# Kernel optimization log

Hardware: AMD Instinct MI355X
Metric: run time of the kernel (lower is better)

## Reference

```python
import jax, jax.numpy as jnp
import numpy as np

B, N, DIM = 4, 2048, 512
HEADS, DIM_HEAD = 8, 64
INNER = HEADS * DIM_HEAD  # 512
EPS = 1e-5
SCALE = DIM_HEAD ** -0.5


def _layernorm(x, g):
    # matches custom LayerNorm: unbiased=False var, no bias term
    mean = jnp.mean(x, axis=-1, keepdims=True)
    var = jnp.var(x, axis=-1, keepdims=True)
    return (x - mean) * jax.lax.rsqrt(var + EPS) * g


def setup_inputs() -> dict:
    key = jax.random.key(0)
    ks = jax.random.split(key, 6)
    x = jax.random.normal(ks[0], (B, N, DIM), dtype=jnp.float32)
    attn_bias = jax.random.normal(ks[1], (HEADS, N, N), dtype=jnp.float32)
    w_q = jax.random.normal(ks[2], (DIM, INNER), dtype=jnp.float32) * 0.02
    w_kv = jax.random.normal(ks[3], (DIM, 2 * DIM_HEAD), dtype=jnp.float32) * 0.02
    w_out = jax.random.normal(ks[4], (INNER, DIM), dtype=jnp.float32) * 0.02
    g_in = jnp.ones((DIM,), dtype=jnp.float32)
    g_out = jnp.ones((DIM,), dtype=jnp.float32)
    return {"x": x, "attn_bias": attn_bias, "w_q": w_q, "w_kv": w_kv,
            "w_out": w_out, "g_in": g_in, "g_out": g_out}


def reference(x, attn_bias, w_q, w_kv, w_out, g_in, g_out):
    b, n, _ = x.shape
    xn = _layernorm(x, g_in)                                  # [b, n, dim]
    q = (xn @ w_q).reshape(b, n, HEADS, DIM_HEAD)
    q = jnp.transpose(q, (0, 2, 1, 3)) * SCALE                # [b, h, n, d]
    kv = xn @ w_kv                                            # [b, n, 2d]
    k, v = jnp.split(kv, 2, axis=-1)                          # each [b, n, d] (multi-query)
    sim = jnp.einsum('bhid,bjd->bhij', q, k) + attn_bias      # [b, h, n, n]
    attn = jax.nn.softmax(sim, axis=-1)
    out = jnp.einsum('bhij,bjd->bhid', attn, v)               # [b, h, n, d]
    out = jnp.transpose(out, (0, 2, 1, 3)).reshape(b, n, INNER)
    out = out @ w_out                                         # [b, n, dim]
    return _layernorm(out, g_out)
```

## Files before the change

### kernel.cpp

```cpp
#include <hip/hip_runtime.h>
#include <hip/hip_bf16.h>

#define B_ 4
#define N_ 2048
#define DIM_ 512
#define HEADS_ 8
#define DHEAD_ 64
#define EPS_ 1e-5f
#define SCALE_ 0.125f

typedef __attribute__((ext_vector_type(8))) short short8;
typedef __attribute__((ext_vector_type(4))) float f32x4;
#define MFMA16(a, b, c) __builtin_amdgcn_mfma_f32_16x16x32_bf16(a, b, c, 0, 0, 0)

__device__ __forceinline__ float bf2f(__hip_bfloat16 v) { return __bfloat162float(v); }
__device__ __forceinline__ float us2f(unsigned short u) {
    __hip_bfloat16 h; *(unsigned short*)&h = u; return bf2f(h);
}
__device__ __forceinline__ float load_in(const void* p, size_t i, int isf32) {
    if (isf32) return ((const float*)p)[i];
    return bf2f(((const __hip_bfloat16*)p)[i]);
}

__device__ __forceinline__ void gload_lds16(const void* g, void* l) {
    __builtin_amdgcn_global_load_lds((const __attribute__((address_space(1))) void*)g,
                                     (__attribute__((address_space(3))) void*)l, 16, 0, 0);
}

__global__ void detect_kernel(const unsigned int* __restrict__ g, int* __restrict__ flag) {
    if (threadIdx.x == 0 && blockIdx.x == 0)
        *flag = (*g == 0x3F800000u) ? 1 : 0;
}

__global__ __launch_bounds__(256) void transpose_w(const void* __restrict__ w,
                                                   __hip_bfloat16* __restrict__ wt,
                                                   int K, int N, const int* __restrict__ flag) {
    int isf32 = *flag;
    int idx = blockIdx.x * 256 + threadIdx.x;
    if (idx >= K * N) return;
    int k = idx / N, n = idx % N;
    wt[(size_t)n * K + k] = __float2bfloat16(load_in(w, idx, isf32));
}

__global__ __launch_bounds__(256) void ln1_kernel(const void* __restrict__ x,
                                                  const void* __restrict__ g,
                                                  __hip_bfloat16* __restrict__ out,
                                                  const int* __restrict__ flag) {
    int isf32 = *flag;
    int row = blockIdx.x;
    int tid = threadIdx.x;
    size_t base = (size_t)row * DIM_;
    float v0 = load_in(x, base + tid, isf32);
    float v1 = load_in(x, base + tid + 256, isf32);
    float s = v0 + v1;
    float sq = v0 * v0 + v1 * v1;
    for (int off = 32; off > 0; off >>= 1) {
        s += __shfl_xor(s, off, 64);
        sq += __shfl_xor(sq, off, 64);
    }
    __shared__ float ls[4], lq[4];
    int wid = tid >> 6;
    if ((tid & 63) == 0) { ls[wid] = s; lq[wid] = sq; }
    __syncthreads();
    s = ls[0] + ls[1] + ls[2] + ls[3];
    sq = lq[0] + lq[1] + lq[2] + lq[3];
    float mean = s * (1.0f / DIM_);
    float var = sq * (1.0f / DIM_) - mean * mean;
    float rstd = rsqrtf(var + EPS_);
    out[base + tid]       = __float2bfloat16((v0 - mean) * rstd * load_in(g, tid, isf32));
    out[base + tid + 256] = __float2bfloat16((v1 - mean) * rstd * load_in(g, tid + 256, isf32));
}

__global__ __launch_bounds__(256) void ln2_kernel(const float* __restrict__ x,
                                                  const void* __restrict__ g,
                                                  void* __restrict__ out,
                                                  const int* __restrict__ flag) {
    int isf32 = *flag;
    int row = blockIdx.x;
    int tid = threadIdx.x;
    const float* xr = x + (size_t)row * DIM_;
    float v0 = xr[tid];
    float v1 = xr[tid + 256];
    float s = v0 + v1;
    float sq = v0 * v0 + v1 * v1;
    for (int off = 32; off > 0; off >>= 1) {
        s += __shfl_xor(s, off, 64);
        sq += __shfl_xor(sq, off, 64);
    }
    __shared__ float ls[4], lq[4];
    int wid = tid >> 6;
    if ((tid & 63) == 0) { ls[wid] = s; lq[wid] = sq; }
    __syncthreads();
    s = ls[0] + ls[1] + ls[2] + ls[3];
    sq = lq[0] + lq[1] + lq[2] + lq[3];
    float mean = s * (1.0f / DIM_);
    float var = sq * (1.0f / DIM_) - mean * mean;
    float rstd = rsqrtf(var + EPS_);
    float r0 = (v0 - mean) * rstd * load_in(g, tid, isf32);
    float r1 = (v1 - mean) * rstd * load_in(g, tid + 256, isf32);
    size_t base = (size_t)row * DIM_;
    if (isf32) {
        ((float*)out)[base + tid] = r0;
        ((float*)out)[base + tid + 256] = r1;
    } else {
        ((__hip_bfloat16*)out)[base + tid] = __float2bfloat16(r0);
        ((__hip_bfloat16*)out)[base + tid + 256] = __float2bfloat16(r1);
    }
}

__global__ __launch_bounds__(256) void gemm_mfma_kv(const __hip_bfloat16* __restrict__ A,
                                                    const __hip_bfloat16* __restrict__ Bt,
                                                    __hip_bfloat16* __restrict__ Kout,
                                                    __hip_bfloat16* __restrict__ VTout,
                                                    int M, int N, int K) {
    __shared__ __align__(16) __hip_bfloat16 As[64][72];
    __shared__ __align__(16) __hip_bfloat16 Bs[64][72];
    int tid = threadIdx.x;
    int lane = tid & 63, wave = tid >> 6;
    int quad = lane >> 4, l15 = lane & 15;
    int wr = (wave & 1) * 32, wc = (wave >> 1) * 32;
    int m0 = blockIdx.y * 64, n0 = blockIdx.x * 64;
    f32x4 acc[2][2] = {};

    for (int k0 = 0; k0 < K; k0 += 64) {
        __syncthreads();
#pragma unroll
        for (int t = 0; t < 2; ++t) {
            int idx = tid + 256 * t;
            int r = idx >> 3, cc = (idx & 7) * 8;
            *(uint4*)&As[r][cc] = *(const uint4*)(A + (size_t)(m0 + r) * K + k0 + cc);
            *(uint4*)&Bs[r][cc] = *(const uint4*)(Bt + (size_t)(n0 + r) * K + k0 + cc);
        }
        __syncthreads();
#pragma unroll
        for (int ks = 0; ks < 2; ++ks) {
            short8 a0 = *(const short8*)&As[wr + l15][ks * 32 + quad * 8];
            short8 a1 = *(const short8*)&As[wr + 16 + l15][ks * 32 + quad * 8];
            short8 b0 = *(const short8*)&Bs[wc + l15][ks * 32 + quad * 8];
            short8 b1 = *(const short8*)&Bs[wc + 16 + l15][ks * 32 + quad * 8];
            acc[0][0] = MFMA16(a0, b0, acc[0][0]);
            acc[0][1] = MFMA16(a0, b1, acc[0][1]);
            acc[1][0] = MFMA16(a1, b0, acc[1][0]);
            acc[1][1] = MFMA16(a1, b1, acc[1][1]);
        }
    }
#pragma unroll
    for (int i = 0; i < 2; ++i)
#pragma unroll
        for (int j = 0; j < 2; ++j)
#pragma unroll
            for (int r = 0; r < 4; ++r) {
                int row = m0 + wr + i * 16 + quad * 4 + r;
                int col = n0 + wc + j * 16 + l15;
                float v = acc[i][j][r];
                if (col < 64)
                    Kout[(size_t)row * 64 + col] = __float2bfloat16(v);
                else
                    VTout[((size_t)((row >> 11) * 64 + (col - 64)) << 11) + (row & 2047)] = __float2bfloat16(v);
            }
}

template <int MODE>
__global__ __launch_bounds__(256) void gemm_mfma128(const __hip_bfloat16* __restrict__ A,
                                                    const __hip_bfloat16* __restrict__ Bt,
                                                    void* __restrict__ Cout,
                                                    int M, int N, int K) {
    __shared__ __align__(1024) char AsL[16384];
    __shared__ __align__(1024) char BsL[8192];
    int tid = threadIdx.x;
    int lane = tid & 63, wave = tid >> 6;
    int quad = lane >> 4, l15 = lane & 15;
    int wr = (wave & 1) * 64, wc = (wave >> 1) * 32;
    int m0 = blockIdx.y * 128, n0 = blockIdx.x * 64;
    f32x4 acc[4][2] = {};

    for (int k0 = 0; k0 < K; k0 += 64) {
        __syncthreads();
#pragma unroll
        for (int t = 0; t < 4; ++t) {
            int idx = t * 256 + tid;
            int r = idx >> 3;
            int c = (idx & 7) ^ (r & 7);
            gload_lds16(A + (size_t)(m0 + r) * K + k0 + c * 8, AsL + t * 4096 + wave * 1024);
        }
#pragma unroll
        for (int t = 0; t < 2; ++t) {
            int idx = t * 256 + tid;
            int r = idx >> 3;
            int c = (idx & 7) ^ (r & 7);
            gload_lds16(Bt + (size_t)(n0 + r) * K + k0 + c * 8, BsL + t * 4096 + wave * 1024);
        }
        __syncthreads();
#pragma unroll
        for (int ks = 0; ks < 2; ++ks) {
            short8 a[4], b[2];
#pragma unroll
            for (int i = 0; i < 4; ++i) {
                int ra = wr + i * 16 + l15;
                a[i] = *(const short8*)(AsL + ra * 128 + (((ks * 4 + quad) ^ (ra & 7)) << 4));
            }
#pragma unroll
            for (int j = 0; j < 2; ++j) {
                int rb = wc + j * 16 + l15;
                b[j] = *(const short8*)(BsL + rb * 128 + (((ks * 4 + quad) ^ (rb & 7)) << 4));
            }
#pragma unroll
            for (int i = 0; i < 4; ++i)
#pragma unroll
                for (int j = 0; j < 2; ++j)
                    acc[i][j] = MFMA16(a[i], b[j], acc[i][j]);
        }
    }
#pragma unroll
    for (int i = 0; i < 4; ++i)
#pragma unroll
        for (int j = 0; j < 2; ++j)
#pragma unroll
            for (int r = 0; r < 4; ++r) {
                int row = m0 + wr + i * 16 + quad * 4 + r;
                int col = n0 + wc + j * 16 + l15;
                float v = acc[i][j][r];
                if (MODE == 0)
                    ((__hip_bfloat16*)Cout)[(size_t)row * N + col] = __float2bfloat16(v * SCALE_);
                else
                    ((float*)Cout)[(size_t)row * N + col] = v;
            }
}

__global__ __launch_bounds__(256, 4) void attn_mfma(const __hip_bfloat16* __restrict__ qb,
                                                    const __hip_bfloat16* __restrict__ kb,
                                                    const __hip_bfloat16* __restrict__ vtb,
                                                    const void* __restrict__ bias,
                                                    __hip_bfloat16* __restrict__ ao,
                                                    const int* __restrict__ flag) {
    int isf32 = *flag;
    __shared__ __align__(1024) char KsPs[17408];
    __shared__ __align__(1024) char Vlin[16384];
    __hip_bfloat16 (*Ps)[136] = (__hip_bfloat16(*)[136])KsPs;

    int tid = threadIdx.x;
    int lane = tid & 63, wave = tid >> 6;
    int quad = lane >> 4, l15 = lane & 15;

    int id = blockIdx.x;
    int xcd = id & 7;
    int sg = id >> 3;
    int b = sg & 3;
    int G = (sg >> 2) * 8 + xcd;
    int h = G >> 5;
    int q0 = (G & 31) * 64;

    int qr = wave * 16;

    const __hip_bfloat16* qrow = qb + (size_t)(b * N_ + q0 + qr + l15) * 512 + h * 64;
    short8 aQ0 = *(const short8*)(qrow + quad * 8);
    short8 aQ1 = *(const short8*)(qrow + 32 + quad * 8);

    float m_i = -INFINITY, l_i = 0.f;
    f32x4 Oacc[4] = {};

    const char* biasp = (const char*)bias;
    const size_t brow = (size_t)h * N_ * N_ + (size_t)(q0 + qr + l15) * N_;
    const __hip_bfloat16* kbase = kb + (size_t)b * N_ * 64;
    const __hip_bfloat16* vbase = vtb + ((size_t)(b * 64) << 11);

    for (int k0 = 0; k0 < N_; k0 += 128) {
        __syncthreads();

#pragma unroll
        for (int t = 0; t < 4; ++t) {
            int idx = t * 256 + tid;
            int r = idx >> 3;
            int c = (idx & 7) ^ (r & 7);
            gload_lds16(kbase + (size_t)(k0 + r) * 64 + c * 8,
                        KsPs + t * 4096 + wave * 1024);
        }
#pragma unroll
        for (int t = 0; t < 4; ++t) {
            int idx = t * 256 + tid;
            int r = idx >> 4;
            int c = (idx & 15) ^ (r & 15);
            gload_lds16(vbase + ((size_t)r << 11) + k0 + c * 8,
                        Vlin + t * 4096 + wave * 1024);
        }
        __syncthreads();

        float bv[8][4];
#pragma unroll
        for (int t = 0; t < 8; ++t) {
            size_t eoff = brow + k0 + t * 16 + quad * 4;
            if (isf32) {
                float4 f = *(const float4*)(biasp + eoff * 4);
                bv[t][0] = f.x; bv[t][1] = f.y; bv[t][2] = f.z; bv[t][3] = f.w;
            } else {
                ushort4 u = *(const ushort4*)(biasp + eoff * 2);
                bv[t][0] = us2f(u.x); bv[t][1] = us2f(u.y);
                bv[t][2] = us2f(u.z); bv[t][3] = us2f(u.w);
            }
        }

        f32x4 Sacc[8] = {};
        __builtin_amdgcn_s_setprio(1);
#pragma unroll
        for (int t = 0; t < 8; ++t) {
            int Rr = t * 16 + l15;
            const char* kr = KsPs + Rr * 128;
            int sw = l15 & 7;
            short8 kf0 = *(const short8*)(kr + ((quad ^ sw) << 4));
            short8 kf1 = *(const short8*)(kr + (((quad + 4) ^ sw) << 4));
            Sacc[t] = MFMA16(kf0, aQ0, Sacc[t]);
            Sacc[t] = MFMA16(kf1, aQ1, Sacc[t]);
        }
        __builtin_amdgcn_s_setprio(0);
        __syncthreads();

        float S[8][4], mt[8];
#pragma unroll
        for (int t = 0; t < 8; ++t) {
#pragma unroll
            for (int r = 0; r < 4; ++r) S[t][r] = Sacc[t][r] + bv[t][r];
            mt[t] = fmaxf(fmaxf(S[t][0], S[t][1]), fmaxf(S[t][2], S[t][3]));
        }
        float rm = fmaxf(fmaxf(fmaxf(mt[0], mt[1]), fmaxf(mt[2], mt[3])),
                         fmaxf(fmaxf(mt[4], mt[5]), fmaxf(mt[6], mt[7])));
        rm = fmaxf(rm, __shfl_xor(rm, 16, 64));
        rm = fmaxf(rm, __shfl_xor(rm, 32, 64));
        float mnew = fmaxf(m_i, rm);
        float st[8];
#pragma unroll
        for (int t = 0; t < 8; ++t) {
#pragma unroll
            for (int r = 0; r < 4; ++r) S[t][r] = __expf(S[t][r] - mnew);
            st[t] = (S[t][0] + S[t][1]) + (S[t][2] + S[t][3]);
        }
        float rs = ((st[0] + st[1]) + (st[2] + st[3])) + ((st[4] + st[5]) + (st[6] + st[7]));
        rs += __shfl_xor(rs, 16, 64);
        rs += __shfl_xor(rs, 32, 64);
        float alpha = __expf(m_i - mnew);
        l_i = l_i * alpha + rs;
        m_i = mnew;

        float al[4];
#pragma unroll
        for (int r = 0; r < 4; ++r) al[r] = __shfl(alpha, quad * 4 + r, 64);
#pragma unroll
        for (int d = 0; d < 4; ++d)
#pragma unroll
            for (int r = 0; r < 4; ++r) Oacc[d][r] *= al[r];

#pragma unroll
        for (int t = 0; t < 8; ++t) {
            ushort4 u;
            __hip_bfloat16 h0 = __float2bfloat16(S[t][0]);
            __hip_bfloat16 h1 = __float2bfloat16(S[t][1]);
            __hip_bfloat16 h2 = __float2bfloat16(S[t][2]);
            __hip_bfloat16 h3 = __float2bfloat16(S[t][3]);
            u.x = *(unsigned short*)&h0; u.y = *(unsigned short*)&h1;
            u.z = *(unsigned short*)&h2; u.w = *(unsigned short*)&h3;
            *(ushort4*)&Ps[qr + l15][t * 16 + quad * 4] = u;
        }

        __builtin_amdgcn_s_setprio(1);
#pragma unroll
        for (int ks = 0; ks < 4; ++ks) {
            short8 aP = *(const short8*)&Ps[qr + l15][ks * 32 + quad * 8];
#pragma unroll
            for (int d = 0; d < 4; ++d) {
                int Rv = d * 16 + l15;
                short8 bV = *(const short8*)(Vlin + Rv * 256 + (((ks * 4 + quad) ^ l15) << 4));
                Oacc[d] = MFMA16(aP, bV, Oacc[d]);
            }
        }
        __builtin_amdgcn_s_setprio(0);
    }

    float li[4];
#pragma unroll
    for (int r = 0; r < 4; ++r) li[r] = 1.0f / __shfl(l_i, quad * 4 + r, 64);
#pragma unroll
    for (int d = 0; d < 4; ++d)
#pragma unroll
        for (int r = 0; r < 4; ++r) {
            float v = Oacc[d][r] * li[r];
            ao[(size_t)(b * N_ + q0 + qr + quad * 4 + r) * 512 + h * 64 + d * 16 + l15] =
                __float2bfloat16(v);
        }
}

extern "C" void kernel_launch(void* const* d_in, const int* in_sizes, int n_in,
                              void* d_out, int out_size, void* d_ws, size_t ws_size,
                              hipStream_t stream) {
    const void* x         = d_in[0];
    const void* attn_bias = d_in[1];
    const void* w_q       = d_in[2];
    const void* w_kv      = d_in[3];
    const void* w_out     = d_in[4];
    const void* g_in      = d_in[5];
    const void* g_out     = d_in[6];

    char* w = (char*)d_ws;
    __hip_bfloat16* xn   = (__hip_bfloat16*)w;
    __hip_bfloat16* qsc  = (__hip_bfloat16*)(w + (8u << 20));
    __hip_bfloat16* ao   = (__hip_bfloat16*)(w + (16u << 20));
    __hip_bfloat16* kbuf = (__hip_bfloat16*)(w + (24u << 20));
    __hip_bfloat16* vtb  = (__hip_bfloat16*)(w + (25u << 20));
    __hip_bfloat16* wqT  = (__hip_bfloat16*)(w + (26u << 20));
    __hip_bfloat16* wkvT = (__hip_bfloat16*)(w + (26u << 20) + 524288);
    __hip_bfloat16* woT  = (__hip_bfloat16*)(w + (26u << 20) + 524288 + 131072);
    int* flag            = (int*)(w + (26u << 20) + 524288 + 131072 + 524288);
    float* pj            = (float*)w;

    const int R = B_ * N_;

    hipLaunchKernelGGL(detect_kernel, dim3(1), dim3(1), 0, stream,
                       (const unsigned int*)g_in, flag);
    hipLaunchKernelGGL(transpose_w, dim3(512 * 512 / 256), dim3(256), 0, stream,
                       w_q, wqT, 512, 512, flag);
    hipLaunchKernelGGL(transpose_w, dim3(512 * 128 / 256), dim3(256), 0, stream,
                       w_kv, wkvT, 512, 128, flag);
    hipLaunchKernelGGL(transpose_w, dim3(512 * 512 / 256), dim3(256), 0, stream,
                       w_out, woT, 512, 512, flag);
    hipLaunchKernelGGL(ln1_kernel, dim3(R), dim3(256), 0, stream, x, g_in, xn, flag);
    hipLaunchKernelGGL(HIP_KERNEL_NAME(gemm_mfma128<0>), dim3(512 / 64, R / 128), dim3(256), 0, stream,
                       xn, wqT, (void*)qsc, R, 512, 512);
    hipLaunchKernelGGL(gemm_mfma_kv, dim3(128 / 64, R / 64), dim3(256), 0, stream,
                       xn, wkvT, kbuf, vtb, R, 128, 512);
    hipLaunchKernelGGL(attn_mfma, dim3(1024), dim3(256), 0, stream,
                       qsc, kbuf, vtb, attn_bias, ao, flag);
    hipLaunchKernelGGL(HIP_KERNEL_NAME(gemm_mfma128<2>), dim3(512 / 64, R / 128), dim3(256), 0, stream,
                       ao, woT, (void*)pj, R, 512, 512);
    hipLaunchKernelGGL(ln2_kernel, dim3(R), dim3(256), 0, stream, pj, g_out, d_out, flag);
}
```

Baseline: 333.2 us.

## Double-buffer GEMM LDS tiles, remap block order, tile weight transpose through LDS

The 128x64 GEMM kernel now double-buffers its A/B LDS tiles, prefetching the next K-slice with global_load_lds while MFMAs run on the current one, and uses one sync per iteration instead of two. Blocks use a 1D grid with M-tiles varying fastest, so consecutive blocks share the same weight columns. The weight transpose kernel goes through a 64x64 LDS tile so both reads and writes are coalesced. The price is double the GEMM LDS footprint, which may lower occupancy, and hard-coded grid mapping that assumes M=8192.

```diff
diff --git a/kernel.cpp b/kernel.cpp
--- a/kernel.cpp
+++ b/kernel.cpp
@@ -36,10 +36,20 @@
                                                    __hip_bfloat16* __restrict__ wt,
                                                    int K, int N, const int* __restrict__ flag) {
     int isf32 = *flag;
-    int idx = blockIdx.x * 256 + threadIdx.x;
-    if (idx >= K * N) return;
-    int k = idx / N, n = idx % N;
-    wt[(size_t)n * K + k] = __float2bfloat16(load_in(w, idx, isf32));
+    __shared__ __hip_bfloat16 tile[64][68];
+    int n0 = blockIdx.x * 64, k0 = blockIdx.y * 64;
+    int c = threadIdx.x & 63, rb = threadIdx.x >> 6;
+#pragma unroll
+    for (int i = 0; i < 16; ++i) {
+        int r = rb + i * 4;
+        tile[r][c] = __float2bfloat16(load_in(w, (size_t)(k0 + r) * N + n0 + c, isf32));
+    }
+    __syncthreads();
+#pragma unroll
+    for (int i = 0; i < 16; ++i) {
+        int r = rb + i * 4;
+        wt[(size_t)(n0 + r) * K + k0 + c] = tile[c][r];
+    }
 }
 
 __global__ __launch_bounds__(256) void ln1_kernel(const void* __restrict__ x,
@@ -165,44 +175,67 @@
                                                     const __hip_bfloat16* __restrict__ Bt,
                                                     void* __restrict__ Cout,
                                                     int M, int N, int K) {
-    __shared__ __align__(1024) char AsL[16384];
-    __shared__ __align__(1024) char BsL[8192];
+    __shared__ __align__(1024) char AsL[2][16384];
+    __shared__ __align__(1024) char BsL[2][8192];
     int tid = threadIdx.x;
     int lane = tid & 63, wave = tid >> 6;
     int quad = lane >> 4, l15 = lane & 15;
     int wr = (wave & 1) * 64, wc = (wave >> 1) * 32;
-    int m0 = blockIdx.y * 128, n0 = blockIdx.x * 64;
+    int id = blockIdx.x;
+    int m0 = (id & 63) * 128, n0 = (id >> 6) * 64;
     f32x4 acc[4][2] = {};
 
-    for (int k0 = 0; k0 < K; k0 += 64) {
-        __syncthreads();
-#pragma unroll
-        for (int t = 0; t < 4; ++t) {
-            int idx = t * 256 + tid;
-            int r = idx >> 3;
-            int c = (idx & 7) ^ (r & 7);
-            gload_lds16(A + (size_t)(m0 + r) * K + k0 + c * 8, AsL + t * 4096 + wave * 1024);
-        }
-#pragma unroll
-        for (int t = 0; t < 2; ++t) {
-            int idx = t * 256 + tid;
-            int r = idx >> 3;
-            int c = (idx & 7) ^ (r & 7);
-            gload_lds16(Bt + (size_t)(n0 + r) * K + k0 + c * 8, BsL + t * 4096 + wave * 1024);
-        }
-        __syncthreads();
+#pragma unroll
+    for (int t = 0; t < 4; ++t) {
+        int idx = t * 256 + tid;
+        int r = idx >> 3;
+        int c = (idx & 7) ^ (r & 7);
+        gload_lds16(A + (size_t)(m0 + r) * K + c * 8, AsL[0] + t * 4096 + wave * 1024);
+    }
+#pragma unroll
+    for (int t = 0; t < 2; ++t) {
+        int idx = t * 256 + tid;
+        int r = idx >> 3;
+        int c = (idx & 7) ^ (r & 7);
+        gload_lds16(Bt + (size_t)(n0 + r) * K + c * 8, BsL[0] + t * 4096 + wave * 1024);
+    }
+    __syncthreads();
+
+#pragma unroll 1
+    for (int kt = 0; kt < K / 64; ++kt) {
+        if (kt + 1 < K / 64) {
+            int kn = (kt + 1) * 64;
+            int nb = (kt + 1) & 1;
+#pragma unroll
+            for (int t = 0; t < 4; ++t) {
+                int idx = t * 256 + tid;
+                int r = idx >> 3;
+                int c = (idx & 7) ^ (r & 7);
+                gload_lds16(A + (size_t)(m0 + r) * K + kn + c * 8,
+                            AsL[nb] + t * 4096 + wave * 1024);
+            }
+#pragma unroll
+            for (int t = 0; t < 2; ++t) {
+                int idx = t * 256 + tid;
+                int r = idx >> 3;
+                int c = (idx & 7) ^ (r & 7);
+                gload_lds16(Bt + (size_t)(n0 + r) * K + kn + c * 8,
+                            BsL[nb] + t * 4096 + wave * 1024);
+            }
+        }
+        int buf = kt & 1;
 #pragma unroll
         for (int ks = 0; ks < 2; ++ks) {
             short8 a[4], b[2];
 #pragma unroll
             for (int i = 0; i < 4; ++i) {
                 int ra = wr + i * 16 + l15;
-                a[i] = *(const short8*)(AsL + ra * 128 + (((ks * 4 + quad) ^ (ra & 7)) << 4));
+                a[i] = *(const short8*)(AsL[buf] + ra * 128 + (((ks * 4 + quad) ^ (ra & 7)) << 4));
             }
 #pragma unroll
             for (int j = 0; j < 2; ++j) {
                 int rb = wc + j * 16 + l15;
-                b[j] = *(const short8*)(BsL + rb * 128 + (((ks * 4 + quad) ^ (rb & 7)) << 4));
+                b[j] = *(const short8*)(BsL[buf] + rb * 128 + (((ks * 4 + quad) ^ (rb & 7)) << 4));
             }
 #pragma unroll
             for (int i = 0; i < 4; ++i)
@@ -210,6 +243,7 @@
                 for (int j = 0; j < 2; ++j)
                     acc[i][j] = MFMA16(a[i], b[j], acc[i][j]);
         }
+        __syncthreads();
     }
 #pragma unroll
     for (int i = 0; i < 4; ++i)
@@ -414,20 +448,20 @@
 
     hipLaunchKernelGGL(detect_kernel, dim3(1), dim3(1), 0, stream,
                        (const unsigned int*)g_in, flag);
-    hipLaunchKernelGGL(transpose_w, dim3(512 * 512 / 256), dim3(256), 0, stream,
+    hipLaunchKernelGGL(transpose_w, dim3(512 / 64, 512 / 64), dim3(256), 0, stream,
                        w_q, wqT, 512, 512, flag);
-    hipLaunchKernelGGL(transpose_w, dim3(512 * 128 / 256), dim3(256), 0, stream,
+    hipLaunchKernelGGL(transpose_w, dim3(128 / 64, 512 / 64), dim3(256), 0, stream,
                        w_kv, wkvT, 512, 128, flag);
-    hipLaunchKernelGGL(transpose_w, dim3(512 * 512 / 256), dim3(256), 0, stream,
+    hipLaunchKernelGGL(transpose_w, dim3(512 / 64, 512 / 64), dim3(256), 0, stream,
                        w_out, woT, 512, 512, flag);
     hipLaunchKernelGGL(ln1_kernel, dim3(R), dim3(256), 0, stream, x, g_in, xn, flag);
-    hipLaunchKernelGGL(HIP_KERNEL_NAME(gemm_mfma128<0>), dim3(512 / 64, R / 128), dim3(256), 0, stream,
+    hipLaunchKernelGGL(HIP_KERNEL_NAME(gemm_mfma128<0>), dim3(512), dim3(256), 0, stream,
                        xn, wqT, (void*)qsc, R, 512, 512);
     hipLaunchKernelGGL(gemm_mfma_kv, dim3(128 / 64, R / 64), dim3(256), 0, stream,
                        xn, wkvT, kbuf, vtb, R, 128, 512);
     hipLaunchKernelGGL(attn_mfma, dim3(1024), dim3(256), 0, stream,
                        qsc, kbuf, vtb, attn_bias, ao, flag);
-    hipLaunchKernelGGL(HIP_KERNEL_NAME(gemm_mfma128<2>), dim3(512 / 64, R / 128), dim3(256), 0, stream,
+    hipLaunchKernelGGL(HIP_KERNEL_NAME(gemm_mfma128<2>), dim3(512), dim3(256), 0, stream,
                        ao, woT, (void*)pj, R, 512, 512);
     hipLaunchKernelGGL(ln2_kernel, dim3(R), dim3(256), 0, stream, pj, g_out, d_out, flag);
 }
```

After: 345.0 us. +3.5%, slower.

## Fuse Q and KV projections, merge weight transposes, vectorize layernorms

Applied to the files above, without the earlier changes.

Merges the three weight-transpose launches into one kernel and lays the Q and KV weights out contiguously, so a single 640-block GEMM computes Q, K and transposed V together. The separate small KV GEMM is dropped. Both layernorms now use one wave per row with 8-element vector loads and stores instead of a 256-thread block with an LDS reduction. The output GEMM is specialized and switched to a 1D grid with M-fastest block ordering. The goal is fewer launches and less memory inefficiency in the small stages; the dominant attention kernel is unchanged.

```diff
diff --git a/kernel.cpp b/kernel.cpp
--- a/kernel.cpp
+++ b/kernel.cpp
@@ -32,14 +32,27 @@
         *flag = (*g == 0x3F800000u) ? 1 : 0;
 }
 
-__global__ __launch_bounds__(256) void transpose_w(const void* __restrict__ w,
-                                                   __hip_bfloat16* __restrict__ wt,
-                                                   int K, int N, const int* __restrict__ flag) {
+__global__ __launch_bounds__(256) void transpose3(const void* __restrict__ wq,
+                                                  const void* __restrict__ wkv,
+                                                  const void* __restrict__ wo,
+                                                  __hip_bfloat16* __restrict__ wqT,
+                                                  __hip_bfloat16* __restrict__ wkvT,
+                                                  __hip_bfloat16* __restrict__ woT,
+                                                  const int* __restrict__ flag) {
     int isf32 = *flag;
     int idx = blockIdx.x * 256 + threadIdx.x;
-    if (idx >= K * N) return;
-    int k = idx / N, n = idx % N;
-    wt[(size_t)n * K + k] = __float2bfloat16(load_in(w, idx, isf32));
+    if (idx < 262144) {
+        int k = idx >> 9, n = idx & 511;
+        wqT[(size_t)n * 512 + k] = __float2bfloat16(load_in(wq, idx, isf32));
+    } else if (idx < 327680) {
+        int i = idx - 262144;
+        int k = i >> 7, n = i & 127;
+        wkvT[(size_t)n * 512 + k] = __float2bfloat16(load_in(wkv, i, isf32));
+    } else if (idx < 589824) {
+        int i = idx - 327680;
+        int k = i >> 9, n = i & 511;
+        woT[(size_t)n * 512 + k] = __float2bfloat16(load_in(wo, i, isf32));
+    }
 }
 
 __global__ __launch_bounds__(256) void ln1_kernel(const void* __restrict__ x,
@@ -47,28 +60,38 @@
                                                   __hip_bfloat16* __restrict__ out,
                                                   const int* __restrict__ flag) {
     int isf32 = *flag;
-    int row = blockIdx.x;
-    int tid = threadIdx.x;
-    size_t base = (size_t)row * DIM_;
-    float v0 = load_in(x, base + tid, isf32);
-    float v1 = load_in(x, base + tid + 256, isf32);
-    float s = v0 + v1;
-    float sq = v0 * v0 + v1 * v1;
+    int row = blockIdx.x * 4 + (threadIdx.x >> 6);
+    int lane = threadIdx.x & 63;
+    size_t base = (size_t)row * DIM_ + lane * 8;
+    float v[8];
+    if (isf32) {
+        float4 f0 = *(const float4*)((const float*)x + base);
+        float4 f1 = *(const float4*)((const float*)x + base + 4);
+        v[0] = f0.x; v[1] = f0.y; v[2] = f0.z; v[3] = f0.w;
+        v[4] = f1.x; v[5] = f1.y; v[6] = f1.z; v[7] = f1.w;
+    } else {
+        short8 s8 = *(const short8*)((const __hip_bfloat16*)x + base);
+#pragma unroll
+        for (int e = 0; e < 8; ++e) v[e] = us2f((unsigned short)s8[e]);
+    }
+    float s = 0.f, sq = 0.f;
+#pragma unroll
+    for (int e = 0; e < 8; ++e) { s += v[e]; sq += v[e] * v[e]; }
     for (int off = 32; off > 0; off >>= 1) {
         s += __shfl_xor(s, off, 64);
         sq += __shfl_xor(sq, off, 64);
     }
-    __shared__ float ls[4], lq[4];
-    int wid = tid >> 6;
-    if ((tid & 63) == 0) { ls[wid] = s; lq[wid] = sq; }
-    __syncthreads();
-    s = ls[0] + ls[1] + ls[2] + ls[3];
-    sq = lq[0] + lq[1] + lq[2] + lq[3];
     float mean = s * (1.0f / DIM_);
     float var = sq * (1.0f / DIM_) - mean * mean;
     float rstd = rsqrtf(var + EPS_);
-    out[base + tid]       = __float2bfloat16((v0 - mean) * rstd * load_in(g, tid, isf32));
-    out[base + tid + 256] = __float2bfloat16((v1 - mean) * rstd * load_in(g, tid + 256, isf32));
+    short8 o;
+#pragma unroll
+    for (int e = 0; e < 8; ++e) {
+        float r = (v[e] - mean) * rstd * load_in(g, lane * 8 + e, isf32);
+        __hip_bfloat16 hb = __float2bfloat16(r);
+        o[e] = *(short*)&hb;
+    }
+    *(short8*)(out + base) = o;
 }
 
 __global__ __launch_bounds__(256) void ln2_kernel(const float* __restrict__ x,
@@ -76,102 +99,56 @@
                                                   void* __restrict__ out,
                                                   const int* __restrict__ flag) {
     int isf32 = *flag;
-    int row = blockIdx.x;
-    int tid = threadIdx.x;
-    const float* xr = x + (size_t)row * DIM_;
-    float v0 = xr[tid];
-    float v1 = xr[tid + 256];
-    float s = v0 + v1;
-    float sq = v0 * v0 + v1 * v1;
+    int row = blockIdx.x * 4 + (threadIdx.x >> 6);
+    int lane = threadIdx.x & 63;
+    size_t base = (size_t)row * DIM_ + lane * 8;
+    float4 f0 = *(const float4*)(x + base);
+    float4 f1 = *(const float4*)(x + base + 4);
+    float v[8] = {f0.x, f0.y, f0.z, f0.w, f1.x, f1.y, f1.z, f1.w};
+    float s = 0.f, sq = 0.f;
+#pragma unroll
+    for (int e = 0; e < 8; ++e) { s += v[e]; sq += v[e] * v[e]; }
     for (int off = 32; off > 0; off >>= 1) {
         s += __shfl_xor(s, off, 64);
         sq += __shfl_xor(sq, off, 64);
     }
-    __shared__ float ls[4], lq[4];
-    int wid = tid >> 6;
-    if ((tid & 63) == 0) { ls[wid] = s; lq[wid] = sq; }
-    __syncthreads();
-    s = ls[0] + ls[1] + ls[2] + ls[3];
-    sq = lq[0] + lq[1] + lq[2] + lq[3];
     float mean = s * (1.0f / DIM_);
     float var = sq * (1.0f / DIM_) - mean * mean;
     float rstd = rsqrtf(var + EPS_);
-    float r0 = (v0 - mean) * rstd * load_in(g, tid, isf32);
-    float r1 = (v1 - mean) * rstd * load_in(g, tid + 256, isf32);
-    size_t base = (size_t)row * DIM_;
+    float r[8];
+#pragma unroll
+    for (int e = 0; e < 8; ++e)
+        r[e] = (v[e] - mean) * rstd * load_in(g, lane * 8 + e, isf32);
     if (isf32) {
-        ((float*)out)[base + tid] = r0;
-        ((float*)out)[base + tid + 256] = r1;
+        float4 o0 = {r[0], r[1], r[2], r[3]};
+        float4 o1 = {r[4], r[5], r[6], r[7]};
+        *(float4*)((float*)out + base) = o0;
+        *(float4*)((float*)out + base + 4) = o1;
     } else {
-        ((__hip_bfloat16*)out)[base + tid] = __float2bfloat16(r0);
-        ((__hip_bfloat16*)out)[base + tid + 256] = __float2bfloat16(r1);
-    }
-}
-
-__global__ __launch_bounds__(256) void gemm_mfma_kv(const __hip_bfloat16* __restrict__ A,
-                                                    const __hip_bfloat16* __restrict__ Bt,
-                                                    __hip_bfloat16* __restrict__ Kout,
-                                                    __hip_bfloat16* __restrict__ VTout,
-                                                    int M, int N, int K) {
-    __shared__ __align__(16) __hip_bfloat16 As[64][72];
-    __shared__ __align__(16) __hip_bfloat16 Bs[64][72];
-    int tid = threadIdx.x;
-    int lane = tid & 63, wave = tid >> 6;
-    int quad = lane >> 4, l15 = lane & 15;
-    int wr = (wave & 1) * 32, wc = (wave >> 1) * 32;
-    int m0 = blockIdx.y * 64, n0 = blockIdx.x * 64;
-    f32x4 acc[2][2] = {};
-
-    for (int k0 = 0; k0 < K; k0 += 64) {
-        __syncthreads();
-#pragma unroll
-        for (int t = 0; t < 2; ++t) {
-            int idx = tid + 256 * t;
-            int r = idx >> 3, cc = (idx & 7) * 8;
-            *(uint4*)&As[r][cc] = *(const uint4*)(A + (size_t)(m0 + r) * K + k0 + cc);
-            *(uint4*)&Bs[r][cc] = *(const uint4*)(Bt + (size_t)(n0 + r) * K + k0 + cc);
-        }
-        __syncthreads();
-#pragma unroll
-        for (int ks = 0; ks < 2; ++ks) {
-            short8 a0 = *(const short8*)&As[wr + l15][ks * 32 + quad * 8];
-            short8 a1 = *(const short8*)&As[wr + 16 + l15][ks * 32 + quad * 8];
-            short8 b0 = *(const short8*)&Bs[wc + l15][ks * 32 + quad * 8];
-            short8 b1 = *(const short8*)&Bs[wc + 16 + l15][ks * 32 + quad * 8];
-            acc[0][0] = MFMA16(a0, b0, acc[0][0]);
-            acc[0][1] = MFMA16(a0, b1, acc[0][1]);
-            acc[1][0] = MFMA16(a1, b0, acc[1][0]);
-            acc[1][1] = MFMA16(a1, b1, acc[1][1]);
-        }
-    }
-#pragma unroll
-    for (int i = 0; i < 2; ++i)
-#pragma unroll
-        for (int j = 0; j < 2; ++j)
-#pragma unroll
-            for (int r = 0; r < 4; ++r) {
-                int row = m0 + wr + i * 16 + quad * 4 + r;
-                int col = n0 + wc + j * 16 + l15;
-                float v = acc[i][j][r];
-                if (col < 64)
-                    Kout[(size_t)row * 64 + col] = __float2bfloat16(v);
-                else
-                    VTout[((size_t)((row >> 11) * 64 + (col - 64)) << 11) + (row & 2047)] = __float2bfloat16(v);
-            }
-}
-
-template <int MODE>
-__global__ __launch_bounds__(256) void gemm_mfma128(const __hip_bfloat16* __restrict__ A,
-                                                    const __hip_bfloat16* __restrict__ Bt,
-                                                    void* __restrict__ Cout,
-                                                    int M, int N, int K) {
+        short8 o;
+#pragma unroll
+        for (int e = 0; e < 8; ++e) {
+            __hip_bfloat16 hb = __float2bfloat16(r[e]);
+            o[e] = *(short*)&hb;
+        }
+        *(short8*)((__hip_bfloat16*)out + base) = o;
+    }
+}
+
+__global__ __launch_bounds__(256) void gemm_qkv(const __hip_bfloat16* __restrict__ A,
+                                                const __hip_bfloat16* __restrict__ Bt,
+                                                __hip_bfloat16* __restrict__ qsc,
+                                                __hip_bfloat16* __restrict__ kbuf,
+                                                __hip_bfloat16* __restrict__ vtb,
+                                                int K) {
     __shared__ __align__(1024) char AsL[16384];
     __shared__ __align__(1024) char BsL[8192];
     int tid = threadIdx.x;
     int lane = tid & 63, wave = tid >> 6;
     int quad = lane >> 4, l15 = lane & 15;
     int wr = (wave & 1) * 64, wc = (wave >> 1) * 32;
-    int m0 = blockIdx.y * 128, n0 = blockIdx.x * 64;
+    int id = blockIdx.x;
+    int m0 = (id & 63) * 128, n0 = (id >> 6) * 64;
     f32x4 acc[4][2] = {};
 
     for (int k0 = 0; k0 < K; k0 += 64) {
@@ -220,10 +197,79 @@
                 int row = m0 + wr + i * 16 + quad * 4 + r;
                 int col = n0 + wc + j * 16 + l15;
                 float v = acc[i][j][r];
-                if (MODE == 0)
-                    ((__hip_bfloat16*)Cout)[(size_t)row * N + col] = __float2bfloat16(v * SCALE_);
-                else
-                    ((float*)Cout)[(size_t)row * N + col] = v;
+                if (col < 512) {
+                    qsc[(size_t)row * 512 + col] = __float2bfloat16(v * SCALE_);
+                } else {
+                    int c = col - 512;
+                    if (c < 64)
+                        kbuf[(size_t)row * 64 + c] = __float2bfloat16(v);
+                    else
+                        vtb[((size_t)((row >> 11) * 64 + (c - 64)) << 11) + (row & 2047)] =
+                            __float2bfloat16(v);
+                }
+            }
+}
+
+__global__ __launch_bounds__(256) void gemm_out(const __hip_bfloat16* __restrict__ A,
+                                                const __hip_bfloat16* __restrict__ Bt,
+                                                float* __restrict__ Cout,
+                                                int N, int K) {
+    __shared__ __align__(1024) char AsL[16384];
+    __shared__ __align__(1024) char BsL[8192];
+    int tid = threadIdx.x;
+    int lane = tid & 63, wave = tid >> 6;
+    int quad = lane >> 4, l15 = lane & 15;
+    int wr = (wave & 1) * 64, wc = (wave >> 1) * 32;
+    int id = blockIdx.x;
+    int m0 = (id & 63) * 128, n0 = (id >> 6) * 64;
+    f32x4 acc[4][2] = {};
+
+    for (int k0 = 0; k0 < K; k0 += 64) {
+        __syncthreads();
+#pragma unroll
+        for (int t = 0; t < 4; ++t) {
+            int idx = t * 256 + tid;
+            int r = idx >> 3;
+            int c = (idx & 7) ^ (r & 7);
+            gload_lds16(A + (size_t)(m0 + r) * K + k0 + c * 8, AsL + t * 4096 + wave * 1024);
+        }
+#pragma unroll
+        for (int t = 0; t < 2; ++t) {
+            int idx = t * 256 + tid;
+            int r = idx >> 3;
+            int c = (idx & 7) ^ (r & 7);
+            gload_lds16(Bt + (size_t)(n0 + r) * K + k0 + c * 8, BsL + t * 4096 + wave * 1024);
+        }
+        __syncthreads();
+#pragma unroll
+        for (int ks = 0; ks < 2; ++ks) {
+            short8 a[4], b[2];
+#pragma unroll
+            for (int i = 0; i < 4; ++i) {
+                int ra = wr + i * 16 + l15;
+                a[i] = *(const short8*)(AsL + ra * 128 + (((ks * 4 + quad) ^ (ra & 7)) << 4));
+            }
+#pragma unroll
+            for (int j = 0; j < 2; ++j) {
+                int rb = wc + j * 16 + l15;
+                b[j] = *(const short8*)(BsL + rb * 128 + (((ks * 4 + quad) ^ (rb & 7)) << 4));
+            }
+#pragma unroll
+            for (int i = 0; i < 4; ++i)
+#pragma unroll
+                for (int j = 0; j < 2; ++j)
+                    acc[i][j] = MFMA16(a[i], b[j], acc[i][j]);
+        }
+    }
+#pragma unroll
+    for (int i = 0; i < 4; ++i)
+#pragma unroll
+        for (int j = 0; j < 2; ++j)
+#pragma unroll
+            for (int r = 0; r < 4; ++r) {
+                int row = m0 + wr + i * 16 + quad * 4 + r;
+                int col = n0 + wc + j * 16 + l15;
+                Cout[(size_t)row * N + col] = acc[i][j][r];
             }
 }
 
@@ -404,30 +450,24 @@
     __hip_bfloat16* ao   = (__hip_bfloat16*)(w + (16u << 20));
     __hip_bfloat16* kbuf = (__hip_bfloat16*)(w + (24u << 20));
     __hip_bfloat16* vtb  = (__hip_bfloat16*)(w + (25u << 20));
-    __hip_bfloat16* wqT  = (__hip_bfloat16*)(w + (26u << 20));
-    __hip_bfloat16* wkvT = (__hip_bfloat16*)(w + (26u << 20) + 524288);
-    __hip_bfloat16* woT  = (__hip_bfloat16*)(w + (26u << 20) + 524288 + 131072);
-    int* flag            = (int*)(w + (26u << 20) + 524288 + 131072 + 524288);
-    float* pj            = (float*)w;
+    __hip_bfloat16* wqkvT = (__hip_bfloat16*)(w + (26u << 20));
+    __hip_bfloat16* wkvT  = wqkvT + (size_t)512 * 512;
+    __hip_bfloat16* woT   = (__hip_bfloat16*)(w + (26u << 20) + 1048576);
+    int* flag             = (int*)(w + (26u << 20) + 1048576 + 524288);
+    float* pj             = (float*)w;
 
     const int R = B_ * N_;
 
     hipLaunchKernelGGL(detect_kernel, dim3(1), dim3(1), 0, stream,
                        (const unsigned int*)g_in, flag);
-    hipLaunchKernelGGL(transpose_w, dim3(512 * 512 / 256), dim3(256), 0, stream,
-                       w_q, wqT, 512, 512, flag);
-    hipLaunchKernelGGL(transpose_w, dim3(512 * 128 / 256), dim3(256), 0, stream,
-                       w_kv, wkvT, 512, 128, flag);
-    hipLaunchKernelGGL(transpose_w, dim3(512 * 512 / 256), dim3(256), 0, stream,
-                       w_out, woT, 512, 512, flag);
-    hipLaunchKernelGGL(ln1_kernel, dim3(R), dim3(256), 0, stream, x, g_in, xn, flag);
-    hipLaunchKernelGGL(HIP_KERNEL_NAME(gemm_mfma128<0>), dim3(512 / 64, R / 128), dim3(256), 0, stream,
-                       xn, wqT, (void*)qsc, R, 512, 512);
-    hipLaunchKernelGGL(gemm_mfma_kv, dim3(128 / 64, R / 64), dim3(256), 0, stream,
-                       xn, wkvT, kbuf, vtb, R, 128, 512);
+    hipLaunchKernelGGL(transpose3, dim3(2304), dim3(256), 0, stream,
+                       w_q, w_kv, w_out, wqkvT, wkvT, woT, flag);
+    hipLaunchKernelGGL(ln1_kernel, dim3(R / 4), dim3(256), 0, stream, x, g_in, xn, flag);
+    hipLaunchKernelGGL(gemm_qkv, dim3(640), dim3(256), 0, stream,
+                       xn, wqkvT, qsc, kbuf, vtb, 512);
     hipLaunchKernelGGL(attn_mfma, dim3(1024), dim3(256), 0, stream,
                        qsc, kbuf, vtb, attn_bias, ao, flag);
-    hipLaunchKernelGGL(HIP_KERNEL_NAME(gemm_mfma128<2>), dim3(512 / 64, R / 128), dim3(256), 0, stream,
-                       ao, woT, (void*)pj, R, 512, 512);
-    hipLaunchKernelGGL(ln2_kernel, dim3(R), dim3(256), 0, stream, pj, g_out, d_out, flag);
-}
+    hipLaunchKernelGGL(gemm_out, dim3(512), dim3(256), 0, stream,
+                       ao, woT, pj, 512, 512);
+    hipLaunchKernelGGL(ln2_kernel, dim3(R / 4), dim3(256), 0, stream, pj, g_out, d_out, flag);
+}
```

New measurement: 323.7 us. 2.9% less time.
